# Kernel tuning notes

Hardware: AMD Instinct MI355X
Metric: run time of the kernel (lower is better)

The kernel has to match this reference:

```python
import jax, jax.numpy as jnp
import numpy as np
import math

NUM_HEADS = 12
SPARSITY = 0.2


def setup_inputs() -> dict:
    key = jax.random.key(0)
    ks = jax.random.split(key, 4)
    B, N, C = 8, 1024, 768
    x = jax.random.normal(ks[0], (B, N, C), dtype=jnp.float32)
    origin = jax.random.normal(ks[1], (B, N, C), dtype=jnp.float32)
    W_qkv = jax.random.normal(ks[2], (C, 3 * C), dtype=jnp.float32) * (C ** -0.5)
    W_proj = jax.random.normal(ks[3], (C, C), dtype=jnp.float32) * (C ** -0.5)
    b_proj = jnp.zeros((C,), dtype=jnp.float32)
    return {"x": x, "origin": origin, "W_qkv": W_qkv, "W_proj": W_proj, "b_proj": b_proj}


def reference(x, origin, W_qkv, W_proj, b_proj):
    B, N, C = x.shape
    H = NUM_HEADS
    hd = C // H
    scale = hd ** -0.5
    # qkv projection (no bias), split into q,k,v of shape [B,H,N,hd]
    qkv = (x @ W_qkv).reshape(B, N, 3, H, hd).transpose(2, 0, 3, 1, 4)
    q, k, v = qkv[0], qkv[1], qkv[2]
    # scaled scores with constant bias log(1 + N/197); bias is constant so softmax unaffected,
    # but keep it for faithfulness (threshold is taken on post-softmax values anyway)
    logits = jnp.einsum('bhqd,bhkd->bhqk', q * scale, k) + math.log(1.0 + N / 197.0)
    attn = jax.nn.softmax(logits, axis=-1)  # [B,H,N,N]
    # global per-batch threshold: keep top sparsity fraction of all H*N*N scores
    total = H * N * N
    k_idx = int(total * SPARSITY) - 1  # index in descending order
    attn_flat = attn.reshape(B, total)
    thr = jnp.sort(attn_flat, axis=-1)[:, total - 1 - k_idx]  # ascending sort, pick k-th largest
    attn = jnp.where(attn >= thr[:, None, None, None], attn, jnp.zeros((), attn.dtype))
    # attention output, merge heads, project, residual
    out = jnp.einsum('bhqk,bhkd->bhqd', attn, v).transpose(0, 2, 1, 3).reshape(B, N, C)
    out = out @ W_proj + b_proj
    return out + origin
```

## Files before the change

kernel.cpp:

```cpp
#include <hip/hip_runtime.h>
#include <hip/hip_bf16.h>

#define BATCH 8
#define SEQ   1024
#define CDIM  768
#define HEADS 12
#define HD    64

#define NB1    2048
#define TMIN2  (-24.0f)
#define W2     (24.0f / (float)NB1)
#define INV_W2 ((float)NB1 / 24.0f)
#define HLSTR  (NB1 + 8)
#define K_SUB  314573u
#define QSCALE 0.18033688011112042f

typedef __attribute__((ext_vector_type(8)))  short bf16x8;
typedef __attribute__((ext_vector_type(4)))  short bf16x4;
typedef __attribute__((ext_vector_type(4)))  float f32x4;
typedef __attribute__((ext_vector_type(16))) float f32x16;
typedef __attribute__((ext_vector_type(4)))  unsigned u32x4;
typedef __attribute__((ext_vector_type(2)))  unsigned u32x2;

#define MFMA16(a, b, c) __builtin_amdgcn_mfma_f32_16x16x32_bf16(a, b, c, 0, 0, 0)
#define MFMA32(a, b, c) __builtin_amdgcn_mfma_f32_32x32x16_bf16(a, b, c, 0, 0, 0)
#define EXP2(x) __builtin_amdgcn_exp2f(x)
#define LOG2(x) __builtin_amdgcn_logf(x)

#define GLOAD_LDS16(gsrc, ldst) \
    __builtin_amdgcn_global_load_lds( \
        (const __attribute__((address_space(1))) void*)(gsrc), \
        (__attribute__((address_space(3))) void*)(ldst), 16, 0, 0)

__device__ inline unsigned cvtpk(float lo, float hi) {
    unsigned r;
    asm("v_cvt_pk_bf16_f32 %0, %1, %2" : "=v"(r) : "v"(lo), "v"(hi));
    return r;
}

__global__ __launch_bounds__(256) void prep_all(const float* __restrict__ x,
                                                const float* __restrict__ Wq,
                                                const float* __restrict__ Wp,
                                                short* __restrict__ xb,
                                                short* __restrict__ wqt,
                                                short* __restrict__ wpt) {
    __shared__ float ls[64][68];
    int bid = blockIdx.x, tid = threadIdx.x;
    if (bid < 3072) {
        int i = bid * 256 + tid;
        float4 a = *reinterpret_cast<const float4*>(&x[(size_t)i * 8]);
        float4 b = *reinterpret_cast<const float4*>(&x[(size_t)i * 8 + 4]);
        u32x4 w = {cvtpk(a.x, a.y), cvtpk(a.z, a.w), cvtpk(b.x, b.y), cvtpk(b.z, b.w)};
        *reinterpret_cast<u32x4*>(&xb[(size_t)i * 8]) = w;
        return;
    }
    const float* in;
    short* out;
    int C, t;
    if (bid < 3504) { t = bid - 3072; in = Wq; out = wqt; C = 2304; }
    else            { t = bid - 3504; in = Wp; out = wpt; C = 768; }
    int r0 = (t % 12) * 64, c0 = (t / 12) * 64;
#pragma unroll
    for (int it = 0; it < 4; ++it) {
        int rr = it * 16 + (tid >> 4);
        int cc = (tid & 15) * 4;
        float4 d = *reinterpret_cast<const float4*>(&in[(size_t)(r0 + rr) * C + c0 + cc]);
        ls[rr][cc + 0] = d.x; ls[rr][cc + 1] = d.y; ls[rr][cc + 2] = d.z; ls[rr][cc + 3] = d.w;
    }
    __syncthreads();
#pragma unroll
    for (int it = 0; it < 2; ++it) {
        int orow = it * 32 + (tid >> 3);
        int oc = (tid & 7) * 8;
        u32x4 w = {cvtpk(ls[oc + 0][orow], ls[oc + 1][orow]),
                   cvtpk(ls[oc + 2][orow], ls[oc + 3][orow]),
                   cvtpk(ls[oc + 4][orow], ls[oc + 5][orow]),
                   cvtpk(ls[oc + 6][orow], ls[oc + 7][orow])};
        *reinterpret_cast<u32x4*>(&out[(size_t)(c0 + orow) * 768 + r0 + oc]) = w;
    }
}

__global__ __launch_bounds__(256) void qkv_mfma(const short* __restrict__ A,
                                                const short* __restrict__ Bt,
                                                __hip_bfloat16* __restrict__ q,
                                                __hip_bfloat16* __restrict__ k,
                                                __hip_bfloat16* __restrict__ vt) {
    const int K = 768;
    __shared__ short As[128 * 64];
    __shared__ short Bs[128 * 64];
    int tM = blockIdx.x * 128, tN = blockIdx.y * 128;
    int tid = threadIdx.x, wave = tid >> 6, lane = tid & 63, lg = lane >> 4, lc = lane & 15;
    int wr = wave >> 1, wc = wave & 1;
    int rsub = lane >> 3;
    int gsw = (lane & 7) ^ (rsub & 7);
    f32x4 acc[4][4] = {};

    for (int kc = 0; kc < K; kc += 64) {
#pragma unroll
        for (int j = 0; j < 4; ++j) {
            int s = wave * 4 + j;
            int row = s * 8 + rsub;
            GLOAD_LDS16(&A[(size_t)(tM + row) * K + kc + gsw * 8], &As[s * 512]);
            GLOAD_LDS16(&Bt[(size_t)(tN + row) * K + kc + gsw * 8], &Bs[s * 512]);
        }
        __syncthreads();
        bf16x8 af[4][2], bfr[4][2];
#pragma unroll
        for (int m4 = 0; m4 < 4; ++m4) {
            int r = wr * 64 + m4 * 16 + lc;
            int sw = (r & 7) << 3;
            af[m4][0] = *(bf16x8*)&As[r * 64 + ((lg * 8) ^ sw)];
            af[m4][1] = *(bf16x8*)&As[r * 64 + ((32 + lg * 8) ^ sw)];
        }
#pragma unroll
        for (int n4 = 0; n4 < 4; ++n4) {
            int r = wc * 64 + n4 * 16 + lc;
            int sw = (r & 7) << 3;
            bfr[n4][0] = *(bf16x8*)&Bs[r * 64 + ((lg * 8) ^ sw)];
            bfr[n4][1] = *(bf16x8*)&Bs[r * 64 + ((32 + lg * 8) ^ sw)];
        }
#pragma unroll
        for (int m4 = 0; m4 < 4; ++m4)
#pragma unroll
            for (int n4 = 0; n4 < 4; ++n4) {
                acc[m4][n4] = MFMA16(af[m4][0], bfr[n4][0], acc[m4][n4]);
                acc[m4][n4] = MFMA16(af[m4][1], bfr[n4][1], acc[m4][n4]);
            }
        __syncthreads();
    }
    int three = tN / 768;
    int cbase = tN - three * 768 + wc * 64;
    if (three == 2) {
#pragma unroll
        for (int m4 = 0; m4 < 4; ++m4) {
            int row0 = tM + wr * 64 + m4 * 16 + lg * 4;
            int b = row0 >> 10, n0 = row0 & 1023;
#pragma unroll
            for (int n4 = 0; n4 < 4; ++n4) {
                int cw = cbase + n4 * 16 + lc;
                int h = cw >> 6, d = cw & 63;
                u32x2 w = {cvtpk(acc[m4][n4][0], acc[m4][n4][1]),
                           cvtpk(acc[m4][n4][2], acc[m4][n4][3])};
                *reinterpret_cast<u32x2*>(
                    &vt[(((size_t)(b * HEADS + h) * 64 + d) << 10) + n0]) = w;
            }
        }
    } else {
        __hip_bfloat16* dst = (three == 0) ? q : k;
#pragma unroll
        for (int m4 = 0; m4 < 4; ++m4)
#pragma unroll
            for (int n4 = 0; n4 < 4; ++n4) {
                int cw = cbase + n4 * 16 + lc;
                int h = cw >> 6, d = cw & 63;
#pragma unroll
                for (int r = 0; r < 4; r += 2) {
                    int row = tM + wr * 64 + m4 * 16 + lg * 4 + r;
                    int b = row >> 10, n = row & 1023;
                    float v0 = acc[m4][n4][r], v1 = acc[m4][n4][r + 1];
                    if (three == 0) { v0 *= QSCALE; v1 *= QSCALE; }
                    unsigned w = cvtpk(v0, v1);
                    size_t base = (((size_t)(b * HEADS + h) << 10) + n) * HD + d;
                    *(unsigned short*)&dst[base] = (unsigned short)w;
                    *(unsigned short*)&dst[base + HD] = (unsigned short)(w >> 16);
                }
            }
    }
}

__global__ __launch_bounds__(256) void stats_mfma(const short* __restrict__ q,
                                                  const short* __restrict__ k,
                                                  float* __restrict__ orow,
                                                  unsigned* __restrict__ hist) {
    __shared__ short kls[8192];
    __shared__ unsigned hl[2 * HLSTR];
    int bid = blockIdx.x;
    int grp = bid & 7;
    int bh = bid >> 3;
    int b = bh / HEADS;
    int tid = threadIdx.x, wave = tid >> 6, lane = tid & 63;
    int ql = lane & 31, h = lane >> 5;
    const short* kbase = k + (size_t)bh * SEQ * HD;
    int qrow0 = grp * 128 + wave * 32;
    const short* qbase = q + ((size_t)bh * SEQ + qrow0) * HD;
    bf16x8 qf[4];
#pragma unroll
    for (int f = 0; f < 4; ++f)
        qf[f] = *(const bf16x8*)&qbase[ql * 64 + f * 16 + h * 8];

    for (int i = tid; i < 2 * HLSTR; i += 256) hl[i] = 0;

    int srow = tid >> 3, scol = (tid & 7) * 8;
    unsigned scache[4][8];

    bf16x8 st[4];
#pragma unroll
    for (int j = 0; j < 4; ++j)
        st[j] = *(const bf16x8*)&kbase[(size_t)(j * 32 + srow) * 64 + scol];
#pragma unroll
    for (int j = 0; j < 4; ++j) {
        int r = j * 32 + srow;
        *(bf16x8*)&kls[r * 64 + (scol ^ ((r & 7) << 3))] = st[j];
    }
    __syncthreads();
    float lsum = 0.f;
#pragma unroll
    for (int c = 0; c < 8; ++c) {
        if (c < 7) {
#pragma unroll
            for (int j = 0; j < 4; ++j)
                st[j] = *(const bf16x8*)&kbase[(size_t)((c + 1) * 128 + j * 32 + srow) * 64 + scol];
        }
#pragma unroll
        for (int kT = 0; kT < 4; ++kT) {
            f32x16 acc = {};
#pragma unroll
            for (int f = 0; f < 4; ++f) {
                int krow = kT * 32 + ql;
                bf16x8 af = *(bf16x8*)&kls[krow * 64 + ((f * 16 + h * 8) ^ ((krow & 7) << 3))];
                acc = MFMA32(af, qf[f], acc);
            }
            if (kT == 0 && (c & 1) == 0) {
#pragma unroll
                for (int i = 0; i < 8; ++i)
                    scache[c >> 1][i] = cvtpk(acc[2 * i], acc[2 * i + 1]);
            }
            float s = 0.f;
#pragma unroll
            for (int r = 0; r < 16; ++r) s += EXP2(acc[r]);
            lsum += s;
        }
        __syncthreads();
        if (c < 7) {
#pragma unroll
            for (int j = 0; j < 4; ++j) {
                int r = j * 32 + srow;
                *(bf16x8*)&kls[r * 64 + (scol ^ ((r & 7) << 3))] = st[j];
            }
            __syncthreads();
        }
    }
    lsum += __shfl_xor(lsum, 32, 64);
    float o = LOG2(lsum);
    if (h == 0) orow[(size_t)bh * SEQ + qrow0 + ql] = o;

    unsigned coff = (lane & 1) * HLSTR;
#pragma unroll
    for (int cc = 0; cc < 4; ++cc)
#pragma unroll
        for (int i = 0; i < 8; ++i) {
            unsigned w = scache[cc][i];
            float s0 = __builtin_bit_cast(float, w << 16);
            float s1 = __builtin_bit_cast(float, w & 0xffff0000u);
            int b0 = (int)((s0 - o) * INV_W2 + (float)NB1);
            int b1 = (int)((s1 - o) * INV_W2 + (float)NB1);
            b0 = b0 < 0 ? 0 : (b0 > NB1 - 1 ? NB1 - 1 : b0);
            b1 = b1 < 0 ? 0 : (b1 > NB1 - 1 ? NB1 - 1 : b1);
            atomicAdd(&hl[coff + b0], 1u);
            atomicAdd(&hl[coff + b1], 1u);
        }
    __syncthreads();
    unsigned* hb = hist + (size_t)b * NB1;
    for (int i = tid; i < NB1; i += 256) {
        unsigned s = hl[i] + hl[HLSTR + i];
        if (s) atomicAdd(&hb[i], s);
    }
}

__global__ __launch_bounds__(256) void find_thr(const unsigned* __restrict__ hist,
                                                float* __restrict__ thr) {
    __shared__ unsigned cs[256];
    int b = blockIdx.x, tid = threadIdx.x;
    const unsigned* hb = hist + (size_t)b * NB1;
    unsigned s = 0;
#pragma unroll
    for (int i = 0; i < 8; ++i) s += hb[tid * 8 + i];
    cs[tid] = s;
    __syncthreads();
    unsigned suf = 0;
    for (int j = tid; j < 256; ++j) suf += cs[j];
    unsigned above = suf - cs[tid];
    if (suf >= K_SUB && above < K_SUB) {
        unsigned acc = above;
        for (int bb = 7; bb >= 0; --bb) {
            acc += hb[tid * 8 + bb];
            if (acc >= K_SUB) {
                thr[b] = TMIN2 + (float)(tid * 8 + bb) * W2;
                break;
            }
        }
    }
}

__global__ __launch_bounds__(256) void pv_mfma(const short* __restrict__ q,
                                               const short* __restrict__ k,
                                               const short* __restrict__ vt,
                                               const float* __restrict__ orow,
                                               const float* __restrict__ thr,
                                               __hip_bfloat16* __restrict__ aout) {
    __shared__ __align__(16) char smem[32768];
    short* klsA = (short*)smem;
    short* klsB = (short*)(smem + 8192);
    short* vlsA = (short*)(smem + 16384);
    short* vlsB = (short*)(smem + 24576);
    float* comb = (float*)smem;

    int bid = blockIdx.x;
    int grp = bid & 15;
    int bh = bid >> 4;
    int b = bh / HEADS, hh = bh % HEADS;
    int tid = threadIdx.x, wave = tid >> 6, lane = tid & 63;
    int ql = lane & 31, h = lane >> 5;
    int rh = wave & 1;
    int kh = wave >> 1;
    const short* kbase = k + (size_t)bh * SEQ * HD;
    const short* vtb = vt + (size_t)bh * HD * SEQ;
    int qrow0 = grp * 64 + rh * 32;
    const short* qbase = q + ((size_t)bh * SEQ + qrow0) * HD;
    bf16x8 qf[4];
#pragma unroll
    for (int f = 0; f < 4; ++f)
        qf[f] = *(const bf16x8*)&qbase[ql * 64 + f * 16 + h * 8];
    float o = orow[(size_t)bh * SEQ + qrow0 + ql];
    float tt = thr[b];
    f32x16 oacc[2] = {};
    f32x16 minus_o;
#pragma unroll
    for (int r = 0; r < 16; ++r) minus_o[r] = -o;

    short* kls = kh ? klsB : klsA;
    short* vls = kh ? vlsB : vlsA;

    int sp = tid >> 7;
    int tl = tid & 127;
    int srow = tl >> 3, scol = (tl & 7) * 8;
    short* skls = sp ? klsB : klsA;
    short* svls = sp ? vlsB : vlsA;

    bf16x8 sk[4], sv[4];
    int cc0 = sp * 8;
#pragma unroll
    for (int j = 0; j < 4; ++j) {
        int r = j * 16 + srow;
        sk[j] = *(const bf16x8*)&kbase[(size_t)(cc0 * 64 + r) * 64 + scol];
        sv[j] = *(const bf16x8*)&vtb[((size_t)r << 10) + cc0 * 64 + scol];
    }
#pragma unroll
    for (int j = 0; j < 4; ++j) {
        int r = j * 16 + srow;
        *(bf16x8*)&skls[r * 64 + (scol ^ ((r & 7) << 3))] = sk[j];
        *(bf16x8*)&svls[r * 64 + (scol ^ ((r & 7) << 3))] = sv[j];
    }
    __syncthreads();

    for (int c = 0; c < 8; ++c) {
        if (c < 7) {
            int cc = sp * 8 + c + 1;
#pragma unroll
            for (int j = 0; j < 4; ++j) {
                int r = j * 16 + srow;
                sk[j] = *(const bf16x8*)&kbase[(size_t)(cc * 64 + r) * 64 + scol];
                sv[j] = *(const bf16x8*)&vtb[((size_t)r << 10) + cc * 64 + scol];
            }
        }
#pragma unroll
        for (int kT = 0; kT < 2; ++kT) {
            f32x16 acc = minus_o;
#pragma unroll
            for (int f = 0; f < 4; ++f) {
                int krow = kT * 32 + ql;
                bf16x8 af = *(bf16x8*)&kls[krow * 64 + ((f * 16 + h * 8) ^ ((krow & 7) << 3))];
                acc = MFMA32(af, qf[f], acc);
            }
            float p[16];
#pragma unroll
            for (int r = 0; r < 16; ++r)
                p[r] = (acc[r] >= tt) ? EXP2(acc[r]) : 0.f;
            unsigned c8[8];
#pragma unroll
            for (int i = 0; i < 8; ++i) c8[i] = cvtpk(p[2 * i], p[2 * i + 1]);
#pragma unroll
            for (int s = 0; s < 2; ++s) {
                unsigned a1 = c8[4 * s],     b1 = c8[4 * s + 2];
                unsigned a2 = c8[4 * s + 1], b2 = c8[4 * s + 3];
                asm("v_permlane32_swap_b32 %0, %1" : "+v"(a1), "+v"(b1));
                asm("v_permlane32_swap_b32 %0, %1" : "+v"(a2), "+v"(b2));
                u32x4 W = {a1, a2, b1, b2};
                bf16x8 pa = __builtin_bit_cast(bf16x8, W);
#pragma unroll
                for (int dt = 0; dt < 2; ++dt) {
                    int vrow = dt * 32 + ql;
                    int vcol = (kT * 32 + s * 16 + h * 8) ^ ((vrow & 7) << 3);
                    bf16x8 vf = *(bf16x8*)&vls[vrow * 64 + vcol];
                    oacc[dt] = MFMA32(pa, vf, oacc[dt]);
                }
            }
        }
        __syncthreads();
        if (c < 7) {
#pragma unroll
            for (int j = 0; j < 4; ++j) {
                int r = j * 16 + srow;
                *(bf16x8*)&skls[r * 64 + (scol ^ ((r & 7) << 3))] = sk[j];
                *(bf16x8*)&svls[r * 64 + (scol ^ ((r & 7) << 3))] = sv[j];
            }
            __syncthreads();
        }
    }

    if (kh == 1) {
#pragma unroll
        for (int dt = 0; dt < 2; ++dt)
#pragma unroll
            for (int r = 0; r < 16; ++r) {
                int crow = (r & 3) + 8 * (r >> 2) + 4 * h;
                comb[(rh * 32 + crow) * 65 + dt * 32 + ql] = oacc[dt][r];
            }
    }
    __syncthreads();
    if (kh == 1) return;
#pragma unroll
    for (int dt = 0; dt < 2; ++dt)
#pragma unroll
        for (int r = 0; r < 16; ++r) {
            int crow = (r & 3) + 8 * (r >> 2) + 4 * h;
            oacc[dt][r] += comb[(rh * 32 + crow) * 65 + dt * 32 + ql];
        }
#pragma unroll
    for (int dt = 0; dt < 2; ++dt)
#pragma unroll
        for (int r = 0; r < 16; r += 2) {
            int qr0 = qrow0 + (r & 3) + 8 * (r >> 2) + 4 * h;
            int qr1 = qrow0 + ((r + 1) & 3) + 8 * ((r + 1) >> 2) + 4 * h;
            unsigned w = cvtpk(oacc[dt][r], oacc[dt][r + 1]);
            *(unsigned short*)&aout[((size_t)b * SEQ + qr0) * CDIM + hh * 64 + dt * 32 + ql] =
                (unsigned short)w;
            *(unsigned short*)&aout[((size_t)b * SEQ + qr1) * CDIM + hh * 64 + dt * 32 + ql] =
                (unsigned short)(w >> 16);
        }
}

__global__ __launch_bounds__(256) void proj_mfma(const short* __restrict__ A,
                                                 const short* __restrict__ Bt,
                                                 const float* __restrict__ bias,
                                                 const float* __restrict__ origin,
                                                 float* __restrict__ out) {
    const int K = 768, NN = 768;
    __shared__ short As[128 * 64];
    __shared__ short Bs[128 * 64];
    int tM = blockIdx.x * 128, tN = blockIdx.y * 128;
    int tid = threadIdx.x, wave = tid >> 6, lane = tid & 63, lg = lane >> 4, lc = lane & 15;
    int wr = wave >> 1, wc = wave & 1;
    int rsub = lane >> 3;
    int gsw = (lane & 7) ^ (rsub & 7);
    f32x4 acc[4][4] = {};

    for (int kc = 0; kc < K; kc += 64) {
#pragma unroll
        for (int j = 0; j < 4; ++j) {
            int s = wave * 4 + j;
            int row = s * 8 + rsub;
            GLOAD_LDS16(&A[(size_t)(tM + row) * K + kc + gsw * 8], &As[s * 512]);
            GLOAD_LDS16(&Bt[(size_t)(tN + row) * K + kc + gsw * 8], &Bs[s * 512]);
        }
        __syncthreads();
        bf16x8 af[4][2], bfr[4][2];
#pragma unroll
        for (int m4 = 0; m4 < 4; ++m4) {
            int r = wr * 64 + m4 * 16 + lc;
            int sw = (r & 7) << 3;
            af[m4][0] = *(bf16x8*)&As[r * 64 + ((lg * 8) ^ sw)];
            af[m4][1] = *(bf16x8*)&As[r * 64 + ((32 + lg * 8) ^ sw)];
        }
#pragma unroll
        for (int n4 = 0; n4 < 4; ++n4) {
            int r = wc * 64 + n4 * 16 + lc;
            int sw = (r & 7) << 3;
            bfr[n4][0] = *(bf16x8*)&Bs[r * 64 + ((lg * 8) ^ sw)];
            bfr[n4][1] = *(bf16x8*)&Bs[r * 64 + ((32 + lg * 8) ^ sw)];
        }
#pragma unroll
        for (int m4 = 0; m4 < 4; ++m4)
#pragma unroll
            for (int n4 = 0; n4 < 4; ++n4) {
                acc[m4][n4] = MFMA16(af[m4][0], bfr[n4][0], acc[m4][n4]);
                acc[m4][n4] = MFMA16(af[m4][1], bfr[n4][1], acc[m4][n4]);
            }
        __syncthreads();
    }
#pragma unroll
    for (int m4 = 0; m4 < 4; ++m4)
#pragma unroll
        for (int n4 = 0; n4 < 4; ++n4)
#pragma unroll
            for (int r = 0; r < 4; ++r) {
                int row = tM + wr * 64 + m4 * 16 + lg * 4 + r;
                int col = tN + wc * 64 + n4 * 16 + lc;
                out[(size_t)row * NN + col] = acc[m4][n4][r] + bias[col] + origin[(size_t)row * NN + col];
            }
}

extern "C" void kernel_launch(void* const* d_in, const int* in_sizes, int n_in,
                              void* d_out, int out_size, void* d_ws, size_t ws_size,
                              hipStream_t stream) {
    const float* x      = (const float*)d_in[0];
    const float* origin = (const float*)d_in[1];
    const float* W_qkv  = (const float*)d_in[2];
    const float* W_proj = (const float*)d_in[3];
    const float* b_proj = (const float*)d_in[4];
    float* out = (float*)d_out;
    char* ws = (char*)d_ws;

    const size_t QKV_ELEMS = (size_t)BATCH * HEADS * SEQ * HD;
    const size_t X_ELEMS   = (size_t)BATCH * SEQ * CDIM;
    size_t off = 0;
    short* xb  = (short*)(ws + off); off += X_ELEMS * 2;
    short* wqt = (short*)(ws + off); off += (size_t)2304 * 768 * 2;
    short* wpt = (short*)(ws + off); off += (size_t)768 * 768 * 2;
    short* q   = (short*)(ws + off); off += QKV_ELEMS * 2;
    short* k   = (short*)(ws + off); off += QKV_ELEMS * 2;
    short* vt  = (short*)(ws + off); off += QKV_ELEMS * 2;
    short* aoutb = (short*)(ws + off); off += QKV_ELEMS * 2;
    float* orow = (float*)(ws + off); off += (size_t)BATCH * HEADS * SEQ * 4;
    unsigned* hist = (unsigned*)(ws + off); off += (size_t)BATCH * NB1 * 4;
    float* thr = (float*)(ws + off); off += 8 * 4;

    hipMemsetAsync(hist, 0, (size_t)BATCH * NB1 * sizeof(unsigned), stream);
    prep_all<<<dim3(3648), 256, 0, stream>>>(x, W_qkv, W_proj, xb, wqt, wpt);
    qkv_mfma<<<dim3(64, 18), 256, 0, stream>>>(xb, wqt,
                                               (__hip_bfloat16*)q, (__hip_bfloat16*)k, (__hip_bfloat16*)vt);
    stats_mfma<<<dim3(BATCH * HEADS * 8), 256, 0, stream>>>(q, k, orow, hist);
    find_thr<<<dim3(BATCH), 256, 0, stream>>>(hist, thr);
    pv_mfma<<<dim3(BATCH * HEADS * 16), 256, 0, stream>>>(q, k, vt, orow, thr,
                                                          (__hip_bfloat16*)aoutb);
    proj_mfma<<<dim3(64, 6), 256, 0, stream>>>(aoutb, wpt, b_proj, origin, out);
}
```

Before: 167.1 us.

## Split key range across wave pairs in stats kernel to double grid size

The stats kernel now launches twice as many blocks, each covering 64 query rows instead of 128. Two wave pairs each process half of the key sequence, staged in separate shared buffers, and their partial exp-sums are combined through shared memory before the log. The aim is more parallelism and occupancy on the many-CU GPU. The cost is twice the K loading per query row and an extra sync. The histogram sample keeps the same key tiles, so the sampled-score set is unchanged.

```diff
diff --git a/kernel.cpp b/kernel.cpp
--- a/kernel.cpp
+++ b/kernel.cpp
@@ -172,16 +172,20 @@
                                                   const short* __restrict__ k,
                                                   float* __restrict__ orow,
                                                   unsigned* __restrict__ hist) {
-    __shared__ short kls[8192];
+    __shared__ short klsA[4096];
+    __shared__ short klsB[4096];
     __shared__ unsigned hl[2 * HLSTR];
+    __shared__ float lsx[2][64];
     int bid = blockIdx.x;
-    int grp = bid & 7;
-    int bh = bid >> 3;
+    int grp = bid & 15;
+    int bh = bid >> 4;
     int b = bh / HEADS;
     int tid = threadIdx.x, wave = tid >> 6, lane = tid & 63;
     int ql = lane & 31, h = lane >> 5;
+    int rh = wave & 1;
+    int kh = wave >> 1;
     const short* kbase = k + (size_t)bh * SEQ * HD;
-    int qrow0 = grp * 128 + wave * 32;
+    int qrow0 = grp * 64 + rh * 32;
     const short* qbase = q + ((size_t)bh * SEQ + qrow0) * HD;
     bf16x8 qf[4];
 #pragma unroll
@@ -190,29 +194,37 @@
 
     for (int i = tid; i < 2 * HLSTR; i += 256) hl[i] = 0;
 
-    int srow = tid >> 3, scol = (tid & 7) * 8;
-    unsigned scache[4][8];
-
-    bf16x8 st[4];
+    short* kls = kh ? klsB : klsA;
+
+    int sp = tid >> 7;
+    int tl = tid & 127;
+    int srow = tl >> 3, scol = (tl & 7) * 8;
+    short* skls = sp ? klsB : klsA;
+
+    bf16x8 sk[4];
+    int cc0 = sp * 8;
 #pragma unroll
     for (int j = 0; j < 4; ++j)
-        st[j] = *(const bf16x8*)&kbase[(size_t)(j * 32 + srow) * 64 + scol];
+        sk[j] = *(const bf16x8*)&kbase[(size_t)(cc0 * 64 + j * 16 + srow) * 64 + scol];
 #pragma unroll
     for (int j = 0; j < 4; ++j) {
-        int r = j * 32 + srow;
-        *(bf16x8*)&kls[r * 64 + (scol ^ ((r & 7) << 3))] = st[j];
-    }
-    __syncthreads();
+        int r = j * 16 + srow;
+        *(bf16x8*)&skls[r * 64 + (scol ^ ((r & 7) << 3))] = sk[j];
+    }
+    __syncthreads();
+
     float lsum = 0.f;
+    unsigned scache[2][8];
 #pragma unroll
     for (int c = 0; c < 8; ++c) {
         if (c < 7) {
+            int cc = sp * 8 + c + 1;
 #pragma unroll
             for (int j = 0; j < 4; ++j)
-                st[j] = *(const bf16x8*)&kbase[(size_t)((c + 1) * 128 + j * 32 + srow) * 64 + scol];
-        }
-#pragma unroll
-        for (int kT = 0; kT < 4; ++kT) {
+                sk[j] = *(const bf16x8*)&kbase[(size_t)(cc * 64 + j * 16 + srow) * 64 + scol];
+        }
+#pragma unroll
+        for (int kT = 0; kT < 2; ++kT) {
             f32x16 acc = {};
 #pragma unroll
             for (int f = 0; f < 4; ++f) {
@@ -220,10 +232,10 @@
                 bf16x8 af = *(bf16x8*)&kls[krow * 64 + ((f * 16 + h * 8) ^ ((krow & 7) << 3))];
                 acc = MFMA32(af, qf[f], acc);
             }
-            if (kT == 0 && (c & 1) == 0) {
+            if (kT == 0 && (c & 3) == 0) {
 #pragma unroll
                 for (int i = 0; i < 8; ++i)
-                    scache[c >> 1][i] = cvtpk(acc[2 * i], acc[2 * i + 1]);
+                    scache[c >> 2][i] = cvtpk(acc[2 * i], acc[2 * i + 1]);
             }
             float s = 0.f;
 #pragma unroll
@@ -234,19 +246,21 @@
         if (c < 7) {
 #pragma unroll
             for (int j = 0; j < 4; ++j) {
-                int r = j * 32 + srow;
-                *(bf16x8*)&kls[r * 64 + (scol ^ ((r & 7) << 3))] = st[j];
+                int r = j * 16 + srow;
+                *(bf16x8*)&skls[r * 64 + (scol ^ ((r & 7) << 3))] = sk[j];
             }
             __syncthreads();
         }
     }
     lsum += __shfl_xor(lsum, 32, 64);
-    float o = LOG2(lsum);
-    if (h == 0) orow[(size_t)bh * SEQ + qrow0 + ql] = o;
+    if (h == 0) lsx[kh][rh * 32 + ql] = lsum;
+    __syncthreads();
+    float o = LOG2(lsx[0][rh * 32 + ql] + lsx[1][rh * 32 + ql]);
+    if (kh == 0 && h == 0) orow[(size_t)bh * SEQ + qrow0 + ql] = o;
 
     unsigned coff = (lane & 1) * HLSTR;
 #pragma unroll
-    for (int cc = 0; cc < 4; ++cc)
+    for (int cc = 0; cc < 2; ++cc)
 #pragma unroll
         for (int i = 0; i < 8; ++i) {
             unsigned w = scache[cc][i];
@@ -529,7 +543,7 @@
     prep_all<<<dim3(3648), 256, 0, stream>>>(x, W_qkv, W_proj, xb, wqt, wpt);
     qkv_mfma<<<dim3(64, 18), 256, 0, stream>>>(xb, wqt,
                                                (__hip_bfloat16*)q, (__hip_bfloat16*)k, (__hip_bfloat16*)vt);
-    stats_mfma<<<dim3(BATCH * HEADS * 8), 256, 0, stream>>>(q, k, orow, hist);
+    stats_mfma<<<dim3(BATCH * HEADS * 16), 256, 0, stream>>>(q, k, orow, hist);
     find_thr<<<dim3(BATCH), 256, 0, stream>>>(hist, thr);
     pv_mfma<<<dim3(BATCH * HEADS * 16), 256, 0, stream>>>(q, k, vt, orow, thr,
                                                           (__hip_bfloat16*)aoutb);
```

Measured after the change: 170.3 us. No clear change (+1.9%).
